# Performance work log

Measured on AMD Instinct MI355X. Metric: run time of the kernel, lower is better.

The kernel has to match this reference:

```python
import jax, jax.numpy as jnp
import numpy as np

B, C, L = 32, 256, 4096

def _bn(x, g, b, m, v, eps=1e-5):
    # x: [B, C, L]; eval-mode batchnorm with running stats
    inv = jax.lax.rsqrt(v + eps)
    return (x - m[None, :, None]) * (inv * g)[None, :, None] + b[None, :, None]

def _ln(x, g, b, eps=1e-6):
    # layernorm over last dim
    mu = jnp.mean(x, axis=-1, keepdims=True)
    var = jnp.mean(jnp.square(x - mu), axis=-1, keepdims=True)
    return (x - mu) * jax.lax.rsqrt(var + eps) * g + b

def _conv1d(x, w, stride=1):
    # x: [B, Cin, L], w: [Cout, Cin, K]
    return jax.lax.conv_general_dilated(
        x, w, window_strides=(stride,), padding=[(1, 1)],
        dimension_numbers=('NCW', 'OIW', 'NCW'))

def _dct2_matrix(n, dtype):
    # scipy.fftpack.dct type-II, norm=None: y[k] = 2*sum_n x[n]*cos(pi*k*(2n+1)/(2N))
    k = jnp.arange(n, dtype=dtype)[:, None]
    m = jnp.arange(n, dtype=dtype)[None, :]
    return 2.0 * jnp.cos(jnp.pi * k * (2.0 * m + 1.0) / (2.0 * n))


def setup_inputs() -> dict:
    key = jax.random.key(0)
    ks = jax.random.split(key, 12)
    s_conv = 1.0 / np.sqrt(C * 3)
    s_fc1 = 1.0 / np.sqrt(C)
    s_fc2 = 1.0 / np.sqrt(2 * C)
    return {
        'x': jax.random.normal(ks[0], (B, C, L), jnp.float32),
        'conv1_w': jax.random.normal(ks[1], (C, C, 3), jnp.float32) * s_conv,
        'bn1_g': jnp.ones((C,), jnp.float32),
        'bn1_b': jnp.zeros((C,), jnp.float32),
        'bn1_m': jax.random.normal(ks[2], (C,), jnp.float32) * 0.1,
        'bn1_v': jax.random.uniform(ks[3], (C,), jnp.float32, 0.5, 1.5),
        'conv2_w': jax.random.normal(ks[4], (C, C, 3), jnp.float32) * s_conv,
        'bn2_g': jnp.ones((C,), jnp.float32),
        'bn2_b': jnp.zeros((C,), jnp.float32),
        'bn2_m': jax.random.normal(ks[5], (C,), jnp.float32) * 0.1,
        'bn2_v': jax.random.uniform(ks[6], (C,), jnp.float32, 0.5, 1.5),
        'fc1_w': jax.random.normal(ks[7], (2 * C, C), jnp.float32) * s_fc1,
        'fc2_w': jax.random.normal(ks[8], (C, 2 * C), jnp.float32) * s_fc2,
        'ln_g': jnp.ones((C,), jnp.float32),
        'ln_b': jnp.zeros((C,), jnp.float32),
    }


def reference(x, conv1_w, bn1_g, bn1_b, bn1_m, bn1_v,
              conv2_w, bn2_g, bn2_b, bn2_m, bn2_v,
              fc1_w, fc2_w, ln_g, ln_b):
    out = _bn(_conv1d(x, conv1_w), bn1_g, bn1_b, bn1_m, bn1_v)
    out = jax.nn.relu(out)
    out = _bn(_conv1d(out, conv2_w), bn2_g, bn2_b, bn2_m, bn2_v)

    # ---- FECAM (faithful to source: DCT-II along the channel axis) ----
    xp = jnp.transpose(out, (0, 2, 1))  # [B, L, C]
    Dm = _dct2_matrix(xp.shape[-1], xp.dtype)  # [C, C]
    freq = jnp.einsum('bln,kn->blk', xp, Dm)   # DCT over channel dim
    sd = _ln(freq, ln_g, ln_b)
    h = jax.nn.relu(jnp.einsum('blc,hc->blh', sd, fc1_w))      # C -> 2C
    fw = jax.nn.sigmoid(jnp.einsum('blh,ch->blc', h, fc2_w))   # 2C -> C
    fw = _ln(fw, ln_g, ln_b)  # same LayerNorm module applied again
    out = jnp.transpose(xp * fw, (0, 2, 1))  # [B, C, L]

    # inplanes == planes, stride == 1 -> identity downsample
    return jax.nn.relu(out + x)
```

## Files before the change

kernel.cpp:

```cpp
#include <hip/hip_runtime.h>
#include <math.h>

#define BB 32
#define CC 256
#define LL 4096

typedef __attribute__((ext_vector_type(8))) short bf16x8;
typedef __attribute__((ext_vector_type(4))) float f32x4;

__device__ __forceinline__ unsigned short f2bf(float f) {
  unsigned u = __float_as_uint(f);
  u = (u + 0x7FFFu + ((u >> 16) & 1u)) >> 16;
  return (unsigned short)u;
}
__device__ __forceinline__ float bf2f(unsigned short v) {
  return __uint_as_float(((unsigned)v) << 16);
}
__device__ __forceinline__ int swz16(int blk) { return blk ^ ((blk >> 3) & 7); }

__device__ __forceinline__ void gload_lds16(const unsigned short* g, unsigned short* l) {
  __builtin_amdgcn_global_load_lds(
      (const __attribute__((address_space(1))) unsigned int*)g,
      (__attribute__((address_space(3))) unsigned int*)l, 16, 0, 0);
}

__global__ void init_bias(const float* __restrict__ g1, const float* __restrict__ b1,
                          const float* __restrict__ m1, const float* __restrict__ v1,
                          const float* __restrict__ g2, const float* __restrict__ b2,
                          const float* __restrict__ m2, const float* __restrict__ v2,
                          float* __restrict__ b1f, float* __restrict__ b2f) {
  int c = threadIdx.x;
  b1f[c] = b1[c] - m1[c] * g1[c] * rsqrtf(v1[c] + 1e-5f);
  b2f[c] = b2[c] - m2[c] * g2[c] * rsqrtf(v2[c] + 1e-5f);
}

__global__ void init_wsw(const float* __restrict__ w1, const float* __restrict__ g1,
                         const float* __restrict__ v1,
                         const float* __restrict__ w2, const float* __restrict__ g2,
                         const float* __restrict__ v2,
                         unsigned short* __restrict__ W1sw, unsigned short* __restrict__ W2sw) {
  int id = blockIdx.x * 256 + threadIdx.x;
  int cv = id / 196608;
  int i = id - cv * 196608;
  int kc3t = i >> 13;
  int kc = kc3t / 3, t = kc3t - 3 * kc;
  int rem = i & 8191;
  int nt = rem >> 9, L = (rem >> 3) & 63, j = i & 7;
  int co = nt * 16 + (L & 15);
  int ci = kc * 32 + ((L >> 4) << 3) + j;
  if (cv == 0) {
    float s = g1[co] * rsqrtf(v1[co] + 1e-5f);
    W1sw[i] = f2bf(w1[(co * 256 + ci) * 3 + t] * s);
  } else {
    float s = g2[co] * rsqrtf(v2[co] + 1e-5f);
    W2sw[i] = f2bf(w2[(co * 256 + ci) * 3 + t] * s);
  }
}

__global__ void init_bsw(const float* __restrict__ fc1, const float* __restrict__ fc2,
                         unsigned short* __restrict__ Bd, unsigned short* __restrict__ B1,
                         unsigned short* __restrict__ B2) {
  int id = blockIdx.x * 256 + threadIdx.x;
  if (id < 65536) {
    int i = id;
    int kc = i >> 13, nt = (i >> 9) & 15, L = (i >> 3) & 63, j = i & 7;
    int n = nt * 16 + (L & 15), k = kc * 32 + (L >> 4) * 8 + j;
    int m = (n * (2 * k + 1)) & 1023;
    float v = 2.0f * cosf(3.14159265358979323846f * (float)m * (1.0f / 512.0f));
    Bd[i] = f2bf(v);
  } else if (id < 65536 + 131072) {
    int i = id - 65536;
    int kc = i >> 14, nt = (i >> 9) & 31, L = (i >> 3) & 63, j = i & 7;
    int n = nt * 16 + (L & 15), k = kc * 32 + (L >> 4) * 8 + j;
    B1[i] = f2bf(fc1[n * 256 + k]);
  } else {
    int i = id - 65536 - 131072;
    int kc = i >> 13, nt = (i >> 9) & 15, L = (i >> 3) & 63, j = i & 7;
    int n = nt * 16 + (L & 15), k = kc * 32 + (L >> 4) * 8 + j;
    B2[i] = f2bf(fc2[n * 512 + k]);
  }
}

__global__ __launch_bounds__(256) void transpose_x(const float* __restrict__ x,
                                                   unsigned short* __restrict__ xT) {
  __shared__ unsigned short ts[64][68];
  const int tid = threadIdx.x;
  const int b = blockIdx.z, ci0 = blockIdx.y << 6, l0 = blockIdx.x << 6;
#pragma unroll
  for (int p = 0; p < 4; ++p) {
    int cc = (p << 4) + (tid >> 4);
    int ll = (tid & 15) << 2;
    float4 v = *(const float4*)&x[((((size_t)b << 8) + ci0 + cc) << 12) + l0 + ll];
    ts[ll + 0][cc] = f2bf(v.x);
    ts[ll + 1][cc] = f2bf(v.y);
    ts[ll + 2][cc] = f2bf(v.z);
    ts[ll + 3][cc] = f2bf(v.w);
  }
  __syncthreads();
#pragma unroll
  for (int p = 0; p < 4; ++p) {
    int idx = tid + (p << 8);
    int row = idx >> 4, ch = idx & 15;
    uint2 v = *(const uint2*)&ts[row][ch << 2];
    *(uint2*)&xT[((((size_t)b << 12) + l0 + row) << 8) + ci0 + (ch << 2)] = v;
  }
}

template <bool RELU, bool FRAGOUT>
__global__ __launch_bounds__(256, 3) void conv_mfma(
    const unsigned short* __restrict__ inT, const unsigned short* __restrict__ Wsw,
    const float* __restrict__ bias, unsigned short* __restrict__ outT) {
  __shared__ char smem[51232];
  unsigned short* xs = (unsigned short*)smem;
  unsigned short* smemB = (unsigned short*)(smem + 34848);
  unsigned short* swz = (unsigned short*)smem;

  const int tid = threadIdx.x;
  const int w = tid >> 6, lane = tid & 63;
  const int g = lane >> 4, c = lane & 15;
  const int l0 = blockIdx.x << 6;
  const int b = blockIdx.y;
  const size_t rowbase = ((size_t)b << 12) + l0;

  for (int idx = tid; idx < 66 * 32; idx += 256) {
    int r = idx >> 5, ch = idx & 31;
    int gl = l0 - 1 + r;
    uint4 v = {0, 0, 0, 0};
    if (gl >= 0 && gl < LL)
      v = *(const uint4*)&inT[((((size_t)b << 12) + gl) << 8) + (ch << 3)];
    *(uint4*)&xs[r * 264 + (ch << 3)] = v;
  }
  __syncthreads();

  f32x4 acc[4][4];
#pragma unroll
  for (int i = 0; i < 4; ++i)
#pragma unroll
    for (int j = 0; j < 4; ++j) acc[i][j] = (f32x4){0.f, 0.f, 0.f, 0.f};

  unsigned short* ls = smemB + (w << 11);
  const unsigned short* gsb = Wsw + (w << 11) + (lane << 3);

  for (int kc = 0; kc < 8; ++kc)
#pragma unroll
    for (int t = 0; t < 3; ++t) {
      const unsigned short* gs = gsb + ((kc * 3 + t) << 13);
      asm volatile("s_waitcnt lgkmcnt(0)" ::: "memory");
      gload_lds16(gs, ls);
      gload_lds16(gs + 512, ls + 512);
      gload_lds16(gs + 1024, ls + 1024);
      gload_lds16(gs + 1536, ls + 1536);
      asm volatile("s_waitcnt vmcnt(0)" ::: "memory");
      __builtin_amdgcn_sched_barrier(0);
      bf16x8 af[4];
#pragma unroll
      for (int mt = 0; mt < 4; ++mt)
        af[mt] = *(const bf16x8*)&xs[(mt * 16 + c + t) * 264 + (kc << 5) + (g << 3)];
#pragma unroll
      for (int nt = 0; nt < 4; ++nt) {
        bf16x8 bfv = *(const bf16x8*)&smemB[((w << 2) + nt) * 512 + (lane << 3)];
#pragma unroll
        for (int mt = 0; mt < 4; ++mt)
          acc[mt][nt] = __builtin_amdgcn_mfma_f32_16x16x32_bf16(af[mt], bfv, acc[mt][nt], 0, 0, 0);
      }
    }
  __syncthreads();

  float pb[4];
#pragma unroll
  for (int nt = 0; nt < 4; ++nt) pb[nt] = bias[(w << 6) + nt * 16 + c];
#pragma unroll
  for (int mt = 0; mt < 4; ++mt)
#pragma unroll
    for (int r = 0; r < 4; ++r) {
      int row = mt * 16 + g * 4 + r;
#pragma unroll
      for (int nt = 0; nt < 4; ++nt) {
        float v = acc[mt][nt][r] + pb[nt];
        if (RELU) v = fmaxf(v, 0.f);
        swz[row * 264 + (w << 6) + nt * 16 + c] = f2bf(v);
      }
    }
  __syncthreads();
  if (!FRAGOUT) {
#pragma unroll
    for (int i = 0; i < 8; ++i) {
      int idx = tid + (i << 8);
      int row = idx >> 5, ch = idx & 31;
      *(uint4*)&outT[((rowbase + row) << 8) + (ch << 3)] = *(const uint4*)&swz[row * 264 + (ch << 3)];
    }
  } else {
    const int MT0 = (int)(rowbase >> 4);
#pragma unroll
    for (int i = 0; i < 8; ++i) {
      int f = tid + (i << 8);
      int mtl = f >> 9, kcl = (f >> 6) & 7, L = f & 63;
      int row = mtl * 16 + (L & 15), k0 = (kcl << 5) + ((L >> 4) << 3);
      uint4 v = *(const uint4*)&swz[row * 264 + k0];
      *(uint4*)&outT[(((size_t)(MT0 + mtl) * 8 + kcl) << 9) + L * 8] = v;
    }
  }
}

__global__ __launch_bounds__(256, 4) void gemm_fused(
    const unsigned short* __restrict__ xp, const unsigned short* __restrict__ Bd,
    const unsigned short* __restrict__ B1, const unsigned short* __restrict__ B2,
    const float* __restrict__ lng, const float* __restrict__ lnb,
    const float* __restrict__ xin, float* __restrict__ outp) {
  __shared__ char smem[40960];
  unsigned short* sdS = (unsigned short*)smem;
  unsigned short* hS = (unsigned short*)(smem + 32768);
  float* ps1 = (float*)(smem + 36864);
  float* ps2 = (float*)(smem + 37888);
  unsigned short* swz = (unsigned short*)smem;

  const int tid = threadIdx.x;
  const int w = tid >> 6;
  const int lane = tid & 63;
  const int g = lane >> 4, c = lane & 15;
  const int MT0 = blockIdx.x << 2;
  const int lsw8 = swz16(lane) * 8;

  float pg[4], pb[4];
#pragma unroll
  for (int nt = 0; nt < 4; ++nt) {
    int col = (w << 6) + nt * 16 + c;
    pg[nt] = lng[col]; pb[nt] = lnb[col];
  }

  {
    f32x4 a0[4][4];
#pragma unroll
    for (int i = 0; i < 4; ++i)
#pragma unroll
      for (int j = 0; j < 4; ++j) a0[i][j] = (f32x4){0.f, 0.f, 0.f, 0.f};

    for (int kc = 0; kc < 8; ++kc) {
      bf16x8 af[4];
#pragma unroll
      for (int mt = 0; mt < 4; ++mt)
        af[mt] = *(const bf16x8*)(xp + (((size_t)(MT0 + mt) << 3) + kc) * 512 + lane * 8);
#pragma unroll
      for (int nt = 0; nt < 4; ++nt) {
        bf16x8 bfv = *(const bf16x8*)(Bd + (((size_t)kc << 4) + (w << 2) + nt) * 512 + lane * 8);
#pragma unroll
        for (int mt = 0; mt < 4; ++mt)
          a0[mt][nt] = __builtin_amdgcn_mfma_f32_16x16x32_bf16(af[mt], bfv, a0[mt][nt], 0, 0, 0);
      }
    }

#pragma unroll
    for (int mt = 0; mt < 4; ++mt)
#pragma unroll
      for (int r = 0; r < 4; ++r) {
        float s1 = 0.f, s2 = 0.f;
#pragma unroll
        for (int nt = 0; nt < 4; ++nt) { float v = a0[mt][nt][r]; s1 += v; s2 += v * v; }
#pragma unroll
        for (int m = 1; m < 16; m <<= 1) { s1 += __shfl_xor(s1, m, 64); s2 += __shfl_xor(s2, m, 64); }
        if (c == 0) {
          ps1[(w << 6) + mt * 16 + g * 4 + r] = s1;
          ps2[(w << 6) + mt * 16 + g * 4 + r] = s2;
        }
      }
    __syncthreads();
#pragma unroll
    for (int mt = 0; mt < 4; ++mt)
#pragma unroll
      for (int r = 0; r < 4; ++r) {
        int row15 = g * 4 + r;
        int rr = mt * 16 + row15;
        float s1 = ps1[rr] + ps1[64 + rr] + ps1[128 + rr] + ps1[192 + rr];
        float s2 = ps2[rr] + ps2[64 + rr] + ps2[128 + rr] + ps2[192 + rr];
        float mu = s1 * (1.f / 256.f);
        float var = s2 * (1.f / 256.f) - mu * mu;
        float inv = __builtin_amdgcn_rsqf(var + 1e-6f);
#pragma unroll
        for (int nt = 0; nt < 4; ++nt) {
          int col = (w << 6) + nt * 16 + c;
          float v = (a0[mt][nt][r] - mu) * inv * pg[nt] + pb[nt];
          int blk = (((col >> 3) & 3) << 4) | row15;
          sdS[((mt << 3) + (col >> 5)) * 512 + swz16(blk) * 8 + (col & 7)] = f2bf(v);
        }
      }
    __syncthreads();
  }

  f32x4 acc[4][4];
#pragma unroll
  for (int i = 0; i < 4; ++i)
#pragma unroll
    for (int j = 0; j < 4; ++j) acc[i][j] = (f32x4){0.f, 0.f, 0.f, 0.f};

  for (int hc = 0; hc < 8; ++hc) {
    f32x4 a1[4];
#pragma unroll
    for (int mt = 0; mt < 4; ++mt) a1[mt] = (f32x4){0.f, 0.f, 0.f, 0.f};
    const unsigned short* b1p = B1 + (size_t)((hc << 2) + w) * 512 + lane * 8;
    for (int kc = 0; kc < 8; ++kc) {
      bf16x8 bfv = *(const bf16x8*)(b1p + (size_t)kc * 16384);
#pragma unroll
      for (int mt = 0; mt < 4; ++mt) {
        bf16x8 af = *(const bf16x8*)&sdS[((mt << 3) + kc) * 512 + lsw8];
        a1[mt] = __builtin_amdgcn_mfma_f32_16x16x32_bf16(af, bfv, a1[mt], 0, 0, 0);
      }
    }
#pragma unroll
    for (int mt = 0; mt < 4; ++mt)
#pragma unroll
      for (int r = 0; r < 4; ++r) {
        int row15 = g * 4 + r;
        float v = fmaxf(a1[mt][r], 0.f);
        int blk = (((((w & 1) << 1) | (c >> 3))) << 4) | row15;
        hS[((mt << 1) + (w >> 1)) * 512 + swz16(blk) * 8 + (c & 7)] = f2bf(v);
      }
    __syncthreads();
#pragma unroll
    for (int kcl = 0; kcl < 2; ++kcl) {
      bf16x8 af2[4];
#pragma unroll
      for (int mt = 0; mt < 4; ++mt)
        af2[mt] = *(const bf16x8*)&hS[((mt << 1) + kcl) * 512 + lsw8];
#pragma unroll
      for (int nt = 0; nt < 4; ++nt) {
        bf16x8 bfv = *(const bf16x8*)(B2 + (size_t)((((hc << 1) + kcl) << 4) + (w << 2) + nt) * 512 +
                                      lane * 8);
#pragma unroll
        for (int mt = 0; mt < 4; ++mt)
          acc[mt][nt] = __builtin_amdgcn_mfma_f32_16x16x32_bf16(af2[mt], bfv, acc[mt][nt], 0, 0, 0);
      }
    }
    __syncthreads();
  }

#pragma unroll
  for (int mt = 0; mt < 4; ++mt)
#pragma unroll
    for (int nt = 0; nt < 4; ++nt)
#pragma unroll
      for (int r = 0; r < 4; ++r)
        acc[mt][nt][r] = __builtin_amdgcn_rcpf(1.f + __expf(-acc[mt][nt][r]));
#pragma unroll
  for (int mt = 0; mt < 4; ++mt)
#pragma unroll
    for (int r = 0; r < 4; ++r) {
      float s1 = 0.f, s2 = 0.f;
#pragma unroll
      for (int nt = 0; nt < 4; ++nt) { float v = acc[mt][nt][r]; s1 += v; s2 += v * v; }
#pragma unroll
      for (int m = 1; m < 16; m <<= 1) { s1 += __shfl_xor(s1, m, 64); s2 += __shfl_xor(s2, m, 64); }
      if (c == 0) {
        ps1[(w << 6) + mt * 16 + g * 4 + r] = s1;
        ps2[(w << 6) + mt * 16 + g * 4 + r] = s2;
      }
    }
  __syncthreads();
  float mu_[4][4], inv_[4][4];
#pragma unroll
  for (int mt = 0; mt < 4; ++mt)
#pragma unroll
    for (int r = 0; r < 4; ++r) {
      int rr = mt * 16 + g * 4 + r;
      float s1 = ps1[rr] + ps1[64 + rr] + ps1[128 + rr] + ps1[192 + rr];
      float s2 = ps2[rr] + ps2[64 + rr] + ps2[128 + rr] + ps2[192 + rr];
      float mu = s1 * (1.f / 256.f);
      float var = s2 * (1.f / 256.f) - mu * mu;
      mu_[mt][r] = mu;
      inv_[mt][r] = __builtin_amdgcn_rsqf(var + 1e-6f);
    }
#pragma unroll
  for (int mt = 0; mt < 4; ++mt)
#pragma unroll
    for (int nt = 0; nt < 4; ++nt) {
      alignas(8) unsigned short tmp[4];
#pragma unroll
      for (int r = 0; r < 4; ++r)
        tmp[r] = f2bf((acc[mt][nt][r] - mu_[mt][r]) * inv_[mt][r] * pg[nt] + pb[nt]);
      int col = (w << 6) + nt * 16 + c;
      *(uint2*)&swz[col * 68 + mt * 16 + g * 4] = *(const uint2*)tmp;
    }
  __syncthreads();
  {
    const int row0 = MT0 << 4;
    const int b = row0 >> 12;
    const int l0 = row0 & 4095;
    const int li = tid & 63, cq = tid >> 6;
    const size_t xbase = (size_t)(MT0 + (li >> 4)) * 4096 + (size_t)(li & 15) * 8;
    const size_t obase = ((size_t)((b << 8) + (cq << 6))) * LL + l0 + li;
#pragma unroll
    for (int i8 = 0; i8 < 8; ++i8) {
      bf16x8 xq = *(const bf16x8*)&xp[xbase + (size_t)((cq << 1) + (i8 >> 2)) * 512 +
                                      (size_t)(i8 & 3) * 128];
#pragma unroll
      for (int j = 0; j < 8; ++j) {
        int ic = (i8 << 3) + j;
        int ccol = (cq << 6) + ic;
        float fwv = bf2f(swz[ccol * 68 + li]);
        float xpv = bf2f((unsigned short)xq[j]);
        size_t o = obase + (size_t)ic * LL;
        float ov = fmaf(xpv, fwv, xin[o]);
        outp[o] = fmaxf(ov, 0.f);
      }
    }
  }
}

extern "C" void kernel_launch(void* const* d_in, const int* in_sizes, int n_in,
                              void* d_out, int out_size, void* d_ws, size_t ws_size,
                              hipStream_t stream) {
  const float* x    = (const float*)d_in[0];
  const float* w1   = (const float*)d_in[1];
  const float* g1   = (const float*)d_in[2];
  const float* b1   = (const float*)d_in[3];
  const float* m1   = (const float*)d_in[4];
  const float* v1   = (const float*)d_in[5];
  const float* w2   = (const float*)d_in[6];
  const float* g2   = (const float*)d_in[7];
  const float* b2   = (const float*)d_in[8];
  const float* m2   = (const float*)d_in[9];
  const float* v2   = (const float*)d_in[10];
  const float* fc1  = (const float*)d_in[11];
  const float* fc2  = (const float*)d_in[12];
  const float* lng  = (const float*)d_in[13];
  const float* lnb  = (const float*)d_in[14];
  float* out = (float*)d_out;

  float* ws = (float*)d_ws;
  float* b1f = ws;
  float* b2f = ws + 256;
  unsigned short* Bd   = (unsigned short*)(ws + 512);
  unsigned short* B1   = (unsigned short*)(ws + 33280);
  unsigned short* B2   = (unsigned short*)(ws + 98816);
  unsigned short* W1sw = (unsigned short*)(ws + 164352);
  unsigned short* W2sw = (unsigned short*)(ws + 262656);
  unsigned short* xT    = (unsigned short*)(ws + 360960);
  unsigned short* y1T  = (unsigned short*)(ws + 17138176);
  unsigned short* xp_sw = (unsigned short*)(ws + 50692608);

  init_bias<<<1, 256, 0, stream>>>(g1, b1, m1, v1, g2, b2, m2, v2, b1f, b2f);
  init_wsw<<<1536, 256, 0, stream>>>(w1, g1, v1, w2, g2, v2, W1sw, W2sw);
  init_bsw<<<1280, 256, 0, stream>>>(fc1, fc2, Bd, B1, B2);

  transpose_x<<<dim3(64, 4, 32), 256, 0, stream>>>(x, xT);

  conv_mfma<true, false><<<dim3(64, 32), 256, 0, stream>>>(xT, W1sw, b1f, y1T);
  conv_mfma<false, true><<<dim3(64, 32), 256, 0, stream>>>(y1T, W2sw, b2f, xp_sw);

  gemm_fused<<<2048, 256, 0, stream>>>(xp_sw, Bd, B1, B2, lng, lnb, x, out);
}
```

Before: 586.3 us.

## Fuse second conv into FECAM GEMM kernel, keeping conv output in LDS

```diff
diff --git a/kernel.cpp b/kernel.cpp
--- a/kernel.cpp
+++ b/kernel.cpp
@@ -106,7 +106,7 @@
   }
 }
 
-template <bool RELU, bool FRAGOUT>
+template <bool RELU>
 __global__ __launch_bounds__(256, 3) void conv_mfma(
     const unsigned short* __restrict__ inT, const unsigned short* __restrict__ Wsw,
     const float* __restrict__ bias, unsigned short* __restrict__ outT) {
@@ -182,44 +182,115 @@
       }
     }
   __syncthreads();
-  if (!FRAGOUT) {
-#pragma unroll
-    for (int i = 0; i < 8; ++i) {
-      int idx = tid + (i << 8);
-      int row = idx >> 5, ch = idx & 31;
-      *(uint4*)&outT[((rowbase + row) << 8) + (ch << 3)] = *(const uint4*)&swz[row * 264 + (ch << 3)];
-    }
-  } else {
-    const int MT0 = (int)(rowbase >> 4);
-#pragma unroll
-    for (int i = 0; i < 8; ++i) {
-      int f = tid + (i << 8);
-      int mtl = f >> 9, kcl = (f >> 6) & 7, L = f & 63;
-      int row = mtl * 16 + (L & 15), k0 = (kcl << 5) + ((L >> 4) << 3);
-      uint4 v = *(const uint4*)&swz[row * 264 + k0];
-      *(uint4*)&outT[(((size_t)(MT0 + mtl) * 8 + kcl) << 9) + L * 8] = v;
-    }
-  }
-}
-
-__global__ __launch_bounds__(256, 4) void gemm_fused(
-    const unsigned short* __restrict__ xp, const unsigned short* __restrict__ Bd,
-    const unsigned short* __restrict__ B1, const unsigned short* __restrict__ B2,
+#pragma unroll
+  for (int i = 0; i < 8; ++i) {
+    int idx = tid + (i << 8);
+    int row = idx >> 5, ch = idx & 31;
+    *(uint4*)&outT[((rowbase + row) << 8) + (ch << 3)] = *(const uint4*)&swz[row * 264 + (ch << 3)];
+  }
+}
+
+__global__ __launch_bounds__(256, 3) void conv2_gemm(
+    const unsigned short* __restrict__ y1T, const unsigned short* __restrict__ W2sw,
+    const float* __restrict__ b2f,
+    const unsigned short* __restrict__ Bd, const unsigned short* __restrict__ B1,
+    const unsigned short* __restrict__ B2,
     const float* __restrict__ lng, const float* __restrict__ lnb,
     const float* __restrict__ xin, float* __restrict__ outp) {
-  __shared__ char smem[40960];
+  __shared__ char smem[51232];
+  unsigned short* xs = (unsigned short*)smem;
+  unsigned short* xpS = (unsigned short*)smem;
   unsigned short* sdS = (unsigned short*)smem;
-  unsigned short* hS = (unsigned short*)(smem + 32768);
-  float* ps1 = (float*)(smem + 36864);
-  float* ps2 = (float*)(smem + 37888);
   unsigned short* swz = (unsigned short*)smem;
+  unsigned short* smemB = (unsigned short*)(smem + 34848);
+  unsigned short* hS = (unsigned short*)(smem + 34848);
+  float* ps1 = (float*)(smem + 43040);
+  float* ps2 = (float*)(smem + 44064);
 
   const int tid = threadIdx.x;
   const int w = tid >> 6;
   const int lane = tid & 63;
   const int g = lane >> 4, c = lane & 15;
   const int MT0 = blockIdx.x << 2;
+  const int b = blockIdx.x >> 6;
+  const int l0 = (blockIdx.x & 63) << 6;
   const int lsw8 = swz16(lane) * 8;
+
+  {
+    for (int idx = tid; idx < 66 * 32; idx += 256) {
+      int r = idx >> 5, ch = idx & 31;
+      int gl = l0 - 1 + r;
+      uint4 v = {0, 0, 0, 0};
+      if (gl >= 0 && gl < LL)
+        v = *(const uint4*)&y1T[((((size_t)b << 12) + gl) << 8) + (ch << 3)];
+      *(uint4*)&xs[r * 264 + (ch << 3)] = v;
+    }
+    __syncthreads();
+
+    f32x4 acc[4][4];
+#pragma unroll
+    for (int i = 0; i < 4; ++i)
+#pragma unroll
+      for (int j = 0; j < 4; ++j) acc[i][j] = (f32x4){0.f, 0.f, 0.f, 0.f};
+
+    unsigned short* ls = smemB + (w << 11);
+    const unsigned short* gsb = W2sw + (w << 11) + (lane << 3);
+
+    for (int kc = 0; kc < 8; ++kc)
+#pragma unroll
+      for (int t = 0; t < 3; ++t) {
+        const unsigned short* gs = gsb + ((kc * 3 + t) << 13);
+        asm volatile("s_waitcnt lgkmcnt(0)" ::: "memory");
+        gload_lds16(gs, ls);
+        gload_lds16(gs + 512, ls + 512);
+        gload_lds16(gs + 1024, ls + 1024);
+        gload_lds16(gs + 1536, ls + 1536);
+        asm volatile("s_waitcnt vmcnt(0)" ::: "memory");
+        __builtin_amdgcn_sched_barrier(0);
+        bf16x8 af[4];
+#pragma unroll
+        for (int mt = 0; mt < 4; ++mt)
+          af[mt] = *(const bf16x8*)&xs[(mt * 16 + c + t) * 264 + (kc << 5) + (g << 3)];
+#pragma unroll
+        for (int nt = 0; nt < 4; ++nt) {
+          bf16x8 bfv = *(const bf16x8*)&smemB[((w << 2) + nt) * 512 + (lane << 3)];
+#pragma unroll
+          for (int mt = 0; mt < 4; ++mt)
+            acc[mt][nt] = __builtin_amdgcn_mfma_f32_16x16x32_bf16(af[mt], bfv, acc[mt][nt], 0, 0, 0);
+        }
+      }
+    __syncthreads();
+
+    float pbc[4];
+#pragma unroll
+    for (int nt = 0; nt < 4; ++nt) pbc[nt] = b2f[(w << 6) + nt * 16 + c];
+#pragma unroll
+    for (int mt = 0; mt < 4; ++mt)
+#pragma unroll
+      for (int r = 0; r < 4; ++r) {
+        int row15 = g * 4 + r;
+#pragma unroll
+        for (int nt = 0; nt < 4; ++nt) {
+          int col = (w << 6) + nt * 16 + c;
+          float v = acc[mt][nt][r] + pbc[nt];
+          int blk = (((col >> 3) & 3) << 4) | row15;
+          xpS[((mt << 3) + (col >> 5)) * 512 + swz16(blk) * 8 + (col & 7)] = f2bf(v);
+        }
+      }
+    __syncthreads();
+  }
+
+  bf16x8 xqr[8];
+  {
+    const int li = tid & 63, cq = tid >> 6;
+    const int mt_ = li >> 4;
+#pragma unroll
+    for (int i8 = 0; i8 < 8; ++i8) {
+      int kcp = (cq << 1) + (i8 >> 2);
+      int blk = ((i8 & 3) << 4) | (li & 15);
+      xqr[i8] = *(const bf16x8*)&xpS[((mt_ << 3) + kcp) * 512 + swz16(blk) * 8];
+    }
+  }
 
   float pg[4], pb[4];
 #pragma unroll
@@ -239,7 +310,7 @@
       bf16x8 af[4];
 #pragma unroll
       for (int mt = 0; mt < 4; ++mt)
-        af[mt] = *(const bf16x8*)(xp + (((size_t)(MT0 + mt) << 3) + kc) * 512 + lane * 8);
+        af[mt] = *(const bf16x8*)&xpS[((mt << 3) + kc) * 512 + lsw8];
 #pragma unroll
       for (int nt = 0; nt < 4; ++nt) {
         bf16x8 bfv = *(const bf16x8*)(Bd + (((size_t)kc << 4) + (w << 2) + nt) * 512 + lane * 8);
@@ -380,17 +451,13 @@
       *(uint2*)&swz[col * 68 + mt * 16 + g * 4] = *(const uint2*)tmp;
     }
   __syncthreads();
+
   {
-    const int row0 = MT0 << 4;
-    const int b = row0 >> 12;
-    const int l0 = row0 & 4095;
     const int li = tid & 63, cq = tid >> 6;
-    const size_t xbase = (size_t)(MT0 + (li >> 4)) * 4096 + (size_t)(li & 15) * 8;
     const size_t obase = ((size_t)((b << 8) + (cq << 6))) * LL + l0 + li;
 #pragma unroll
     for (int i8 = 0; i8 < 8; ++i8) {
-      bf16x8 xq = *(const bf16x8*)&xp[xbase + (size_t)((cq << 1) + (i8 >> 2)) * 512 +
-                                      (size_t)(i8 & 3) * 128];
+      bf16x8 xq = xqr[i8];
 #pragma unroll
       for (int j = 0; j < 8; ++j) {
         int ic = (i8 << 3) + j;
@@ -433,9 +500,8 @@
   unsigned short* B2   = (unsigned short*)(ws + 98816);
   unsigned short* W1sw = (unsigned short*)(ws + 164352);
   unsigned short* W2sw = (unsigned short*)(ws + 262656);
-  unsigned short* xT    = (unsigned short*)(ws + 360960);
+  unsigned short* xT   = (unsigned short*)(ws + 360960);
   unsigned short* y1T  = (unsigned short*)(ws + 17138176);
-  unsigned short* xp_sw = (unsigned short*)(ws + 50692608);
 
   init_bias<<<1, 256, 0, stream>>>(g1, b1, m1, v1, g2, b2, m2, v2, b1f, b2f);
   init_wsw<<<1536, 256, 0, stream>>>(w1, g1, v1, w2, g2, v2, W1sw, W2sw);
@@ -443,8 +509,7 @@
 
   transpose_x<<<dim3(64, 4, 32), 256, 0, stream>>>(x, xT);
 
-  conv_mfma<true, false><<<dim3(64, 32), 256, 0, stream>>>(xT, W1sw, b1f, y1T);
-  conv_mfma<false, true><<<dim3(64, 32), 256, 0, stream>>>(y1T, W2sw, b2f, xp_sw);
-
-  gemm_fused<<<2048, 256, 0, stream>>>(xp_sw, Bd, B1, B2, lng, lnb, x, out);
-}
+  conv_mfma<true><<<dim3(64, 32), 256, 0, stream>>>(xT, W1sw, b1f, y1T);
+
+  conv2_gemm<<<2048, 256, 0, stream>>>(y1T, W2sw, b2f, Bd, B1, B2, lng, lnb, x, out);
+}
```

Measured after the change: 584.4 us. Within noise of the previous version (-0.3%).
